# Kernel tuning notes

Measured on AMD Instinct MI355X. Metric: run time of the kernel, lower is better.

Reference implementation:

```python
import jax, jax.numpy as jnp
import numpy as np
import hashlib

MAX_HASH_VALUE = 2 ** 8  # 256
BATCH, MAX_LEN, EMB, HID, VOCAB = 32, 512, 256, 1024, 32000


def _hash_mod(flat_ids, algo):
    # SHA digest interpreted little-endian; only value mod 256 matters for the
    # downstream (h1 + k*h2) % 256, and mod 256 of a little-endian int is just
    # the first digest byte. We keep the full int.from_bytes for faithfulness.
    return np.array(
        [int.from_bytes(algo(str(int(v)).encode()).digest(), 'little') % MAX_HASH_VALUE
         for v in flat_ids],
        dtype=np.int64,
    )


def setup_inputs() -> dict:
    key = jax.random.key(0)
    k1, k2, k3 = jax.random.split(key, 3)
    input_ids = jax.random.randint(k1, (BATCH, MAX_LEN), 0, VOCAB, dtype=jnp.int64)
    W = jax.random.normal(k2, (HID, EMB), dtype=jnp.float32) * (1.0 / np.sqrt(EMB))
    b = jax.random.normal(k3, (HID,), dtype=jnp.float32) * 0.01
    return {"input_ids": input_ids, "W": W, "b": b}


def reference(input_ids, W, b):
    ids = np.asarray(input_ids)            # [B, L] int
    B, L = ids.shape
    flat = ids.reshape(-1)
    h1 = _hash_mod(flat, hashlib.sha256).reshape(B, L)   # [B, L] in [0,256)
    h2 = _hash_mod(flat, hashlib.sha224).reshape(B, L)
    k = jnp.arange(EMB, dtype=jnp.int64)                 # [E]
    # hash3[b,l,k] = (h1 + k*h2) % 256
    hash3 = ((jnp.asarray(h1)[:, :, None] + k[None, None, :] * jnp.asarray(h2)[:, :, None])
             % MAX_HASH_VALUE).astype(jnp.float32)        # [B, L, E]
    out = jnp.einsum('ble,he->blh', hash3, W) + b        # [B, L, H]
    return out
```

## Files before the change

### kernel.cpp

```cpp
#include <hip/hip_runtime.h>
#include <stdint.h>

typedef short bf16x8 __attribute__((ext_vector_type(8)));
typedef float f32x16 __attribute__((ext_vector_type(16)));
typedef float f32x4 __attribute__((ext_vector_type(4)));
typedef unsigned short ushort_t;

#define EMB 256
#define HID 1024
#define NTOK 16384

#define WS_W_OFF 0
#define WS_H_OFF (512u * 1024u)

#define ROTR(x,n) (((x)>>(n))|((x)<<(32-(n))))
#define S0F(x) (ROTR((x),7)^ROTR((x),18)^((x)>>3))
#define S1F(x) (ROTR((x),17)^ROTR((x),19)^((x)>>10))

#define RND1(Kc, Wt) do {                                                          \
    uint32_t t1_ = sh + (ROTR(se,6)^ROTR(se,11)^ROTR(se,25))                       \
                   + ((se&sf)^(~se&sg)) + (Kc) + (Wt);                             \
    uint32_t t2_ = (ROTR(sa,2)^ROTR(sa,13)^ROTR(sa,22))                            \
                   + ((sa&sb)^(sa&sc)^(sb&sc));                                    \
    sh=sg; sg=sf; sf=se; se=sd+t1_; sd=sc; sc=sb; sb=sa; sa=t1_+t2_; } while (0)

#define WSXS(a,b,c,d) ((a) += S0F(b) + (c) + S1F(d))

__device__ __forceinline__ uint32_t rbf(float x) {
    uint32_t b = __float_as_uint(x);
    return (b + 0x7FFFu + ((b >> 16) & 1u)) >> 16;
}
__device__ __forceinline__ uint4 pack8(float4 a, float4 b) {
    uint4 q;
    q.x = rbf(a.x) | (rbf(a.y) << 16);
    q.y = rbf(a.z) | (rbf(a.w) << 16);
    q.z = rbf(b.x) | (rbf(b.y) << 16);
    q.w = rbf(b.z) | (rbf(b.w) << 16);
    return q;
}

#define MFMA(av,bv,acc) __builtin_amdgcn_mfma_f32_32x32x16_bf16(av,bv,acc,0,0,0)

__global__ __launch_bounds__(128) void prep_kernel(const uint32_t* __restrict__ ids32,
                                                   const float* __restrict__ W,
                                                   ushort_t* __restrict__ Wf,
                                                   ushort_t* __restrict__ Hs) {
    __shared__ uint32_t redf[2];
    const int tid = (int)threadIdx.x;
    const int g = (int)blockIdx.x * 128 + tid;

    const int h = g >> 5, c8 = g & 31, kk = c8 >> 1, h8 = c8 & 1;
    const float4* wsrc = reinterpret_cast<const float4*>(W + h * EMB + kk * 16 + h8 * 8);
    float4 wa = wsrc[0], wb = wsrc[1];

    {
        const uint4* ids4 = reinterpret_cast<const uint4*>(ids32);
        uint4 da = ids4[tid], db = ids4[tid + 128];
        uint32_t z = da.y | da.w | db.y | db.w;
        unsigned long long m = __ballot(z != 0u);
        if ((tid & 63) == 0) redf[tid >> 6] = (m != 0ull) ? 1u : 0u;
    }
    __syncthreads();
    const bool is64 = (redf[0] | redf[1]) == 0u;

    const int tok = g >> 1;
    const uint32_t st = g & 1;
    const uint32_t v = is64 ? ids32[2 * tok] : ids32[tok];

    const uint32_t q4 = __umulhi(v, 0xD1B71759u) >> 13;
    const uint32_t r4 = v - q4 * 10000u;
    const uint32_t q3 = __umulhi(r4, 0x10624DD3u) >> 6;
    const uint32_t r3 = r4 - q3 * 1000u;
    const uint32_t q2 = __umulhi(r3, 0x51EB851Fu) >> 5;
    const uint32_t r2 = r3 - q2 * 100u;
    const uint32_t q1 = __umulhi(r2, 0xCCCCCCCDu) >> 3;
    const uint32_t q0 = r2 - q1 * 10u;
    const uint32_t nd = v >= 10000u ? 5u : v >= 1000u ? 4u : v >= 100u ? 3u
                         : v >= 10u ? 2u : 1u;
    uint64_t M = ((uint64_t)(q4 + '0') << 56) | ((uint64_t)(q3 + '0') << 48) |
                 ((uint64_t)(q2 + '0') << 40) | ((uint64_t)(q1 + '0') << 32) |
                 ((uint64_t)(q0 + '0') << 24) | ((uint64_t)0x80u << 16);
    M <<= 8u * (5u - nd);

    uint32_t w0 = (uint32_t)(M >> 32), w1 = (uint32_t)M;
    uint32_t w2 = 0, w3 = 0, w4 = 0, w5 = 0, w6 = 0, w7 = 0;
    uint32_t w8 = 0, w9 = 0, w10 = 0, w11 = 0, w12 = 0, w13 = 0, w14 = 0;
    uint32_t w15 = nd * 8u;

    uint32_t sa = st ? 0xc1059ed8u : 0x6a09e667u;
    uint32_t sb = st ? 0x367cd507u : 0xbb67ae85u;
    uint32_t sc = st ? 0x3070dd17u : 0x3c6ef372u;
    uint32_t sd = st ? 0xf70e5939u : 0xa54ff53au;
    uint32_t se = st ? 0xffc00b31u : 0x510e527fu;
    uint32_t sf = st ? 0x68581511u : 0x9b05688cu;
    uint32_t sg = st ? 0x64f98fa7u : 0x1f83d9abu;
    uint32_t sh = st ? 0xbefa4fa4u : 0x5be0cd19u;

    RND1(0x428a2f98u, w0);  RND1(0x71374491u, w1);  RND1(0xb5c0fbcfu, w2);
    RND1(0xe9b5dba5u, w3);  RND1(0x3956c25bu, w4);  RND1(0x59f111f1u, w5);
    RND1(0x923f82a4u, w6);  RND1(0xab1c5ed5u, w7);  RND1(0xd807aa98u, w8);
    RND1(0x12835b01u, w9);  RND1(0x243185beu, w10); RND1(0x550c7dc3u, w11);
    RND1(0x72be5d74u, w12); RND1(0x80deb1feu, w13); RND1(0x9bdc06a7u, w14);
    RND1(0xc19bf174u, w15);
    WSXS(w0,w1,w9,w14);    RND1(0xe49b69c1u, w0);
    WSXS(w1,w2,w10,w15);   RND1(0xefbe4786u, w1);
    WSXS(w2,w3,w11,w0);    RND1(0x0fc19dc6u, w2);
    WSXS(w3,w4,w12,w1);    RND1(0x240ca1ccu, w3);
    WSXS(w4,w5,w13,w2);    RND1(0x2de92c6fu, w4);
    WSXS(w5,w6,w14,w3);    RND1(0x4a7484aau, w5);
    WSXS(w6,w7,w15,w4);    RND1(0x5cb0a9dcu, w6);
    WSXS(w7,w8,w0,w5);     RND1(0x76f988dau, w7);
    WSXS(w8,w9,w1,w6);     RND1(0x983e5152u, w8);
    WSXS(w9,w10,w2,w7);    RND1(0xa831c66du, w9);
    WSXS(w10,w11,w3,w8);   RND1(0xb00327c8u, w10);
    WSXS(w11,w12,w4,w9);   RND1(0xbf597fc7u, w11);
    WSXS(w12,w13,w5,w10);  RND1(0xc6e00bf3u, w12);
    WSXS(w13,w14,w6,w11);  RND1(0xd5a79147u, w13);
    WSXS(w14,w15,w7,w12);  RND1(0x06ca6351u, w14);
    WSXS(w15,w0,w8,w13);   RND1(0x14292967u, w15);
    WSXS(w0,w1,w9,w14);    RND1(0x27b70a85u, w0);
    WSXS(w1,w2,w10,w15);   RND1(0x2e1b2138u, w1);
    WSXS(w2,w3,w11,w0);    RND1(0x4d2c6dfcu, w2);
    WSXS(w3,w4,w12,w1);    RND1(0x53380d13u, w3);
    WSXS(w4,w5,w13,w2);    RND1(0x650a7354u, w4);
    WSXS(w5,w6,w14,w3);    RND1(0x766a0abbu, w5);
    WSXS(w6,w7,w15,w4);    RND1(0x81c2c92eu, w6);
    WSXS(w7,w8,w0,w5);     RND1(0x92722c85u, w7);
    WSXS(w8,w9,w1,w6);     RND1(0xa2bfe8a1u, w8);
    WSXS(w9,w10,w2,w7);    RND1(0xa81a664bu, w9);
    WSXS(w10,w11,w3,w8);   RND1(0xc24b8b70u, w10);
    WSXS(w11,w12,w4,w9);   RND1(0xc76c51a3u, w11);
    WSXS(w12,w13,w5,w10);  RND1(0xd192e819u, w12);
    WSXS(w13,w14,w6,w11);  RND1(0xd6990624u, w13);
    WSXS(w14,w15,w7,w12);  RND1(0xf40e3585u, w14);
    WSXS(w15,w0,w8,w13);   RND1(0x106aa070u, w15);
    WSXS(w0,w1,w9,w14);    RND1(0x19a4c116u, w0);
    WSXS(w1,w2,w10,w15);   RND1(0x1e376c08u, w1);
    WSXS(w2,w3,w11,w0);    RND1(0x2748774cu, w2);
    WSXS(w3,w4,w12,w1);    RND1(0x34b0bcb5u, w3);
    WSXS(w4,w5,w13,w2);    RND1(0x391c0cb3u, w4);
    WSXS(w5,w6,w14,w3);    RND1(0x4ed8aa4au, w5);
    WSXS(w6,w7,w15,w4);    RND1(0x5b9cca4fu, w6);
    WSXS(w7,w8,w0,w5);     RND1(0x682e6ff3u, w7);
    WSXS(w8,w9,w1,w6);     RND1(0x748f82eeu, w8);
    WSXS(w9,w10,w2,w7);    RND1(0x78a5636fu, w9);
    WSXS(w10,w11,w3,w8);   RND1(0x84c87814u, w10);
    WSXS(w11,w12,w4,w9);   RND1(0x8cc70208u, w11);
    WSXS(w12,w13,w5,w10);  RND1(0x90befffau, w12);
    WSXS(w13,w14,w6,w11);  RND1(0xa4506cebu, w13);
    WSXS(w14,w15,w7,w12);  RND1(0xbef9a3f7u, w14);
    WSXS(w15,w0,w8,w13);   RND1(0xc67178f2u, w15);

    const uint32_t hv = ((st ? 0xc1059ed8u : 0x6a09e667u) + sa) >> 24;
    const uint32_t hvo = __shfl_xor(hv, 1);
    if (st == 0) Hs[tok] = (ushort_t)(hv | (hvo << 8));

    const int P = h >> 7, hl = h & 127, j = hl & 3, cc = hl >> 2;
    uint4* wbase = reinterpret_cast<uint4*>(Wf)
                   + ((size_t)(P * 4 + j) * 16 + kk) * 64 + cc + h8 * 32;
    *wbase = pack8(wa, wb);
}

__global__ __launch_bounds__(256, 2) void fused_kernel(const ushort_t* __restrict__ Hs,
                                                       const ushort_t* __restrict__ Wf,
                                                       const float* __restrict__ bias,
                                                       float* __restrict__ out) {
    __shared__ uint4 Albuf[4096];

    const int bid = blockIdx.x;
    const int bm = bid >> 2;
    const int nb0 = (bid & 3) * 256;
    const int tid = (int)threadIdx.x;
    const int wv = tid >> 6, lane = tid & 63, lrow = lane & 31, lh = lane >> 5;
    const int wm = wv >> 1;
    const int wn2 = wv & 1;

    {
        const int rr = tid >> 1;
        const uint32_t st = tid & 1;
        const uint32_t hsv = Hs[bm * 128 + rr];
        const uint32_t hv1 = hsv & 255u, hv2 = hsv >> 8;
        const int ag = rr >> 5, aslot = rr & 31;
        uint32_t val = (hv1 + (st ? ((hv2 << 7) & 255u) : 0u)) & 255u;
        const int kfb = (int)st * 8;
#define PAIR(dst) { uint32_t lo_ = val; uint32_t hi_ = (val + hv2) & 255u;        \
                    val = (hi_ + hv2) & 255u;                                     \
                    dst = (__float_as_uint((float)lo_) >> 16) |                   \
                          (__float_as_uint((float)hi_) & 0xFFFF0000u); }
#pragma unroll
        for (int q = 0; q < 8; ++q) {
            uint32_t c0_, c1_, c2_, c3_, c4_, c5_, c6_, c7_;
            PAIR(c0_); PAIR(c1_); PAIR(c2_); PAIR(c3_);
            PAIR(c4_); PAIR(c5_); PAIR(c6_); PAIR(c7_);
            uint4 qa; qa.x = c0_; qa.y = c1_; qa.z = c2_; qa.w = c3_;
            uint4 qb; qb.x = c4_; qb.y = c5_; qb.z = c6_; qb.w = c7_;
            Albuf[(ag * 16 + kfb + q) * 64 + aslot]      = qa;
            Albuf[(ag * 16 + kfb + q) * 64 + aslot + 32] = qb;
        }
#undef PAIR
    }

    const int C0 = nb0 + wn2 * 128;
    const f32x4 b4 = *reinterpret_cast<const f32x4*>(bias + C0 + 4 * lrow);

    __syncthreads();

    const bf16x8* bfr = reinterpret_cast<const bf16x8*>(Wf);
    const bf16x8* alr = reinterpret_cast<const bf16x8*>(Albuf);
    const int gb0 = (C0 >> 7) * 4;
    const int agA0 = (wm * 2) * 16, agA1 = (wm * 2 + 1) * 16;

    f32x16 A00 = (f32x16)(0.0f), A01 = (f32x16)(0.0f);
    f32x16 A02 = (f32x16)(0.0f), A03 = (f32x16)(0.0f);
    f32x16 A10 = (f32x16)(0.0f), A11 = (f32x16)(0.0f);
    f32x16 A12 = (f32x16)(0.0f), A13 = (f32x16)(0.0f);

#pragma unroll 2
    for (int kf = 0; kf < 16; ++kf) {
        bf16x8 av0 = alr[(agA0 + kf) * 64 + lane];
        bf16x8 av1 = alr[(agA1 + kf) * 64 + lane];
        bf16x8 bv0 = bfr[((size_t)((gb0 + 0) * 16 + kf)) * 64 + lane];
        bf16x8 bv1 = bfr[((size_t)((gb0 + 1) * 16 + kf)) * 64 + lane];
        bf16x8 bv2 = bfr[((size_t)((gb0 + 2) * 16 + kf)) * 64 + lane];
        bf16x8 bv3 = bfr[((size_t)((gb0 + 3) * 16 + kf)) * 64 + lane];
        A00 = MFMA(av0, bv0, A00); A01 = MFMA(av0, bv1, A01);
        A02 = MFMA(av0, bv2, A02); A03 = MFMA(av0, bv3, A03);
        A10 = MFMA(av1, bv0, A10); A11 = MFMA(av1, bv1, A11);
        A12 = MFMA(av1, bv2, A12); A13 = MFMA(av1, bv3, A13);
    }

    const int m0 = bm * 128 + wm * 64;
    float* obase = out + (size_t)C0 + 4 * lrow;
#pragma unroll
    for (int r = 0; r < 16; ++r) {
        const int rowl = (r & 3) + 8 * (r >> 2) + 4 * lh;
        f32x4 v0, v1;
        v0[0] = A00[r] + b4[0]; v0[1] = A01[r] + b4[1];
        v0[2] = A02[r] + b4[2]; v0[3] = A03[r] + b4[3];
        v1[0] = A10[r] + b4[0]; v1[1] = A11[r] + b4[1];
        v1[2] = A12[r] + b4[2]; v1[3] = A13[r] + b4[3];
        __builtin_nontemporal_store(
            v0, reinterpret_cast<f32x4*>(obase + (size_t)(m0 + rowl) * HID));
        __builtin_nontemporal_store(
            v1, reinterpret_cast<f32x4*>(obase + (size_t)(m0 + 32 + rowl) * HID));
    }
}

extern "C" void kernel_launch(void* const* d_in, const int* in_sizes, int n_in,
                              void* d_out, int out_size, void* d_ws, size_t ws_size,
                              hipStream_t stream) {
    const uint32_t* ids32 = (const uint32_t*)d_in[0];
    const float* W = (const float*)d_in[1];
    const float* bias = (const float*)d_in[2];
    float* out = (float*)d_out;
    ushort_t* Wf = (ushort_t*)((char*)d_ws + WS_W_OFF);
    ushort_t* Hs = (ushort_t*)((char*)d_ws + WS_H_OFF);
    (void)in_sizes; (void)n_in; (void)out_size; (void)ws_size;

    prep_kernel<<<256, 128, 0, stream>>>(ids32, W, Wf, Hs);
    fused_kernel<<<512, 256, 0, stream>>>(Hs, Wf, bias, out);
}
```

Baseline: 32.92 us.

## Retile fused GEMM to 64-row blocks covering full HID with 8 waves

Each block now handles 64 token rows and all 1024 output columns using 512 threads (8 waves, one 128-column strip each), instead of 128 rows by 256 columns with 4 waves. The A-tile generation is split across 8 threads per token, so the hash-expanded bf16 tile is built once per row block rather than four times across column blocks. Output stores switch from nontemporal to regular stores. This halves the grid to 256 blocks and raises per-block thread count, which may change occupancy and W fragment reuse.

```diff
diff --git a/kernel.cpp b/kernel.cpp
--- a/kernel.cpp
+++ b/kernel.cpp
@@ -161,54 +161,52 @@
     *wbase = pack8(wa, wb);
 }
 
-__global__ __launch_bounds__(256, 2) void fused_kernel(const ushort_t* __restrict__ Hs,
+__global__ __launch_bounds__(512, 2) void fused_kernel(const ushort_t* __restrict__ Hs,
                                                        const ushort_t* __restrict__ Wf,
                                                        const float* __restrict__ bias,
                                                        float* __restrict__ out) {
-    __shared__ uint4 Albuf[4096];
-
-    const int bid = blockIdx.x;
-    const int bm = bid >> 2;
-    const int nb0 = (bid & 3) * 256;
+    __shared__ uint4 Albuf[2048];
+
+    const int bm = (int)blockIdx.x;
     const int tid = (int)threadIdx.x;
     const int wv = tid >> 6, lane = tid & 63, lrow = lane & 31, lh = lane >> 5;
-    const int wm = wv >> 1;
-    const int wn2 = wv & 1;
 
     {
-        const int rr = tid >> 1;
-        const uint32_t st = tid & 1;
-        const uint32_t hsv = Hs[bm * 128 + rr];
+        const int tk = tid >> 3;
+        const int sub = tid & 7;
+        const uint32_t st = (uint32_t)(sub >> 2);
+        const int qh = sub & 3;
+        const uint32_t hsv = Hs[bm * 64 + tk];
         const uint32_t hv1 = hsv & 255u, hv2 = hsv >> 8;
-        const int ag = rr >> 5, aslot = rr & 31;
-        uint32_t val = (hv1 + (st ? ((hv2 << 7) & 255u) : 0u)) & 255u;
-        const int kfb = (int)st * 8;
+        const int ag = tk >> 5, aslot = tk & 31;
+        const uint32_t kstart = st * 128u + (uint32_t)qh * 32u;
+        uint32_t val = (hv1 + hv2 * kstart) & 255u;
+        const int kf0 = (int)st * 8 + qh * 2;
 #define PAIR(dst) { uint32_t lo_ = val; uint32_t hi_ = (val + hv2) & 255u;        \
                     val = (hi_ + hv2) & 255u;                                     \
                     dst = (__float_as_uint((float)lo_) >> 16) |                   \
                           (__float_as_uint((float)hi_) & 0xFFFF0000u); }
 #pragma unroll
-        for (int q = 0; q < 8; ++q) {
+        for (int q = 0; q < 2; ++q) {
             uint32_t c0_, c1_, c2_, c3_, c4_, c5_, c6_, c7_;
             PAIR(c0_); PAIR(c1_); PAIR(c2_); PAIR(c3_);
             PAIR(c4_); PAIR(c5_); PAIR(c6_); PAIR(c7_);
             uint4 qa; qa.x = c0_; qa.y = c1_; qa.z = c2_; qa.w = c3_;
             uint4 qb; qb.x = c4_; qb.y = c5_; qb.z = c6_; qb.w = c7_;
-            Albuf[(ag * 16 + kfb + q) * 64 + aslot]      = qa;
-            Albuf[(ag * 16 + kfb + q) * 64 + aslot + 32] = qb;
+            Albuf[(ag * 16 + kf0 + q) * 64 + aslot]      = qa;
+            Albuf[(ag * 16 + kf0 + q) * 64 + aslot + 32] = qb;
         }
 #undef PAIR
     }
 
-    const int C0 = nb0 + wn2 * 128;
+    const int C0 = wv * 128;
     const f32x4 b4 = *reinterpret_cast<const f32x4*>(bias + C0 + 4 * lrow);
 
     __syncthreads();
 
     const bf16x8* bfr = reinterpret_cast<const bf16x8*>(Wf);
     const bf16x8* alr = reinterpret_cast<const bf16x8*>(Albuf);
-    const int gb0 = (C0 >> 7) * 4;
-    const int agA0 = (wm * 2) * 16, agA1 = (wm * 2 + 1) * 16;
+    const int gb0 = wv * 4;
 
     f32x16 A00 = (f32x16)(0.0f), A01 = (f32x16)(0.0f);
     f32x16 A02 = (f32x16)(0.0f), A03 = (f32x16)(0.0f);
@@ -217,8 +215,8 @@
 
 #pragma unroll 2
     for (int kf = 0; kf < 16; ++kf) {
-        bf16x8 av0 = alr[(agA0 + kf) * 64 + lane];
-        bf16x8 av1 = alr[(agA1 + kf) * 64 + lane];
+        bf16x8 av0 = alr[kf * 64 + lane];
+        bf16x8 av1 = alr[(16 + kf) * 64 + lane];
         bf16x8 bv0 = bfr[((size_t)((gb0 + 0) * 16 + kf)) * 64 + lane];
         bf16x8 bv1 = bfr[((size_t)((gb0 + 1) * 16 + kf)) * 64 + lane];
         bf16x8 bv2 = bfr[((size_t)((gb0 + 2) * 16 + kf)) * 64 + lane];
@@ -229,7 +227,7 @@
         A12 = MFMA(av1, bv2, A12); A13 = MFMA(av1, bv3, A13);
     }
 
-    const int m0 = bm * 128 + wm * 64;
+    const int m0 = bm * 64;
     float* obase = out + (size_t)C0 + 4 * lrow;
 #pragma unroll
     for (int r = 0; r < 16; ++r) {
@@ -239,10 +237,8 @@
         v0[2] = A02[r] + b4[2]; v0[3] = A03[r] + b4[3];
         v1[0] = A10[r] + b4[0]; v1[1] = A11[r] + b4[1];
         v1[2] = A12[r] + b4[2]; v1[3] = A13[r] + b4[3];
-        __builtin_nontemporal_store(
-            v0, reinterpret_cast<f32x4*>(obase + (size_t)(m0 + rowl) * HID));
-        __builtin_nontemporal_store(
-            v1, reinterpret_cast<f32x4*>(obase + (size_t)(m0 + 32 + rowl) * HID));
+        *reinterpret_cast<f32x4*>(obase + (size_t)(m0 + rowl) * HID)      = v0;
+        *reinterpret_cast<f32x4*>(obase + (size_t)(m0 + 32 + rowl) * HID) = v1;
     }
 }
 
@@ -258,5 +254,5 @@
     (void)in_sizes; (void)n_in; (void)out_size; (void)ws_size;
 
     prep_kernel<<<256, 128, 0, stream>>>(ids32, W, Wf, Hs);
-    fused_kernel<<<512, 256, 0, stream>>>(Hs, Wf, bias, out);
-}
+    fused_kernel<<<256, 512, 0, stream>>>(Hs, Wf, bias, out);
+}
```

After: 32.68 us, median of 2. Within noise of the previous version (-0.7%).
